# Kernel tuning notes

Measured on AMD Instinct MI355X. Metric: run time of the kernel, lower is better.

Reference implementation:

```python
import jax, jax.numpy as jnp
import numpy as np

THRESH = 0.05
MAX_PER_IMAGE = 50
NMS_THRESH = 0.3
BBOX_STD = jnp.array([0.1, 0.1, 0.2, 0.2], dtype=jnp.float32)  # TRAIN.BBOX_NORMALIZE_STDS


def _decode_boxes(rois, deltas, im_info):
    """bbox_transform_inv + clip_boxes + rescale. rois [N,5], deltas [N,4C], im_info [3]=(h,w,scale).
    Returns [N,C,4] boxes in original-image coordinates."""
    boxes = rois[:, 1:5]
    w = boxes[:, 2] - boxes[:, 0] + 1.0
    h = boxes[:, 3] - boxes[:, 1] + 1.0
    cx = boxes[:, 0] + 0.5 * w
    cy = boxes[:, 1] + 0.5 * h
    d = deltas.reshape(deltas.shape[0], -1, 4) * BBOX_STD  # [N,C,4] (unnormalize deltas)
    dx, dy, dw, dh = d[..., 0], d[..., 1], d[..., 2], d[..., 3]
    pcx = dx * w[:, None] + cx[:, None]
    pcy = dy * h[:, None] + cy[:, None]
    pw = jnp.exp(dw) * w[:, None]
    ph = jnp.exp(dh) * h[:, None]
    x1 = jnp.clip(pcx - 0.5 * pw, 0.0, im_info[1] - 1.0)
    y1 = jnp.clip(pcy - 0.5 * ph, 0.0, im_info[0] - 1.0)
    x2 = jnp.clip(pcx + 0.5 * pw, 0.0, im_info[1] - 1.0)
    y2 = jnp.clip(pcy + 0.5 * ph, 0.0, im_info[0] - 1.0)
    return jnp.stack([x1, y1, x2, y2], axis=-1) / im_info[2]


def _nms(boxes, scores, valid):
    """Greedy NMS, fixed shapes. boxes [N,4], scores [N], valid bool [N].
    Returns (boxes_sorted [N,4], kept_scores [N] with -inf for dropped)."""
    n = boxes.shape[0]
    masked = jnp.where(valid, scores, -jnp.inf)
    order = jnp.argsort(-masked)
    b = boxes[order]
    s = masked[order]
    v = valid[order]
    x1, y1, x2, y2 = b[:, 0], b[:, 1], b[:, 2], b[:, 3]
    area = (x2 - x1 + 1.0) * (y2 - y1 + 1.0)
    ix1 = jnp.maximum(x1[:, None], x1[None, :])
    iy1 = jnp.maximum(y1[:, None], y1[None, :])
    ix2 = jnp.minimum(x2[:, None], x2[None, :])
    iy2 = jnp.minimum(y2[:, None], y2[None, :])
    iw = jnp.clip(ix2 - ix1 + 1.0, 0.0)
    ih = jnp.clip(iy2 - iy1 + 1.0, 0.0)
    inter = iw * ih
    iou = inter / (area[:, None] + area[None, :] - inter)  # [N,N]

    def step(keep, i):
        suppressed = jnp.any(keep & (iou[:, i] > NMS_THRESH))
        k = v[i] & jnp.logical_not(suppressed)
        return keep.at[i].set(k), k

    keep, _ = jax.lax.scan(step, jnp.zeros((n,), dtype=bool), jnp.arange(n))
    return b, jnp.where(keep, s, -jnp.inf)


def _per_image(rois, cls_prob, bbox_pred, im_info):
    """select_boxes for one image: decode, threshold, per-class NMS, global top max_per_image.
    Returns per-class best box [C-1,4] and best score [C-1] within the capped detection set."""
    boxes = _decode_boxes(rois, bbox_pred, im_info)  # [N,C,4]
    n, c = cls_prob.shape
    fg = c - 1

    def per_class(cb, cs):
        return _nms(cb, cs, cs > THRESH)

    fb, fs = jax.vmap(per_class, in_axes=(1, 1))(boxes[:, 1:, :], cls_prob[:, 1:])  # [C-1,N,4],[C-1,N]
    flat_s = fs.reshape(-1)
    flat_b = fb.reshape(-1, 4)
    topk_s, idx = jax.lax.top_k(flat_s, MAX_PER_IMAGE)  # global cap at max_per_image
    topk_b = flat_b[idx]
    topk_cls = idx // n  # fg class id of each kept detection
    # per-class best among kept detections (used by select_box)
    onehot = topk_cls[:, None] == jnp.arange(fg)[None, :]  # [max,fg]
    per_cls = jnp.where(onehot, topk_s[:, None], -jnp.inf)  # [max,fg]
    best_s = per_cls.max(axis=0)  # [fg]
    best_b = topk_b[per_cls.argmax(axis=0)]  # [fg,4]
    return best_b, best_s


def _select_boxes(rois, cls_prob, bbox_pred, im_infos):
    return jax.lax.map(lambda t: _per_image(*t), (rois, cls_prob, bbox_pred, im_infos))


def _forward(rois_A, cls_prob_A, bbox_pred_A, im_info_A, rois_B, cls_prob_B, bbox_pred_B, im_info_B):
    bA_b, bA_s = _select_boxes(rois_A, cls_prob_A, bbox_pred_A, im_info_A)  # [B,fg,4],[B,fg]
    bB_b, bB_s = _select_boxes(rois_B, cls_prob_B, bbox_pred_B, im_info_B)
    joint = bA_s * bB_s  # class must score well in BOTH images
    cls = jnp.argmax(joint, axis=1)  # [B]
    bidx = jnp.arange(joint.shape[0])
    box_A = jax.lax.stop_gradient(bA_b[bidx, cls])
    box_B = jax.lax.stop_gradient(bB_b[bidx, cls])
    return box_A, box_B


def setup_inputs() -> dict:
    key = jax.random.key(0)
    ks = jax.random.split(key, 6)
    B, N, C = 8, 2000, 21
    H, W = 600.0, 800.0

    def make_rois(k):
        k1, k2 = jax.random.split(k)
        xy = jax.random.uniform(k1, (B, N, 2)) * jnp.array([W - 1.0, H - 1.0])
        wh = jax.random.uniform(k2, (B, N, 2), minval=8.0, maxval=300.0)
        x2y2 = jnp.minimum(xy + wh, jnp.array([W - 1.0, H - 1.0]))
        bidx = jnp.zeros((B, N, 1))
        return jnp.concatenate([bidx, xy, x2y2], axis=-1).astype(jnp.float32)

    rois_A = make_rois(ks[0])
    rois_B = make_rois(ks[1])
    cls_prob_A = jax.nn.softmax(2.0 * jax.random.normal(ks[2], (B, N, C)), axis=-1).astype(jnp.float32)
    cls_prob_B = jax.nn.softmax(2.0 * jax.random.normal(ks[3], (B, N, C)), axis=-1).astype(jnp.float32)
    bbox_pred_A = (0.2 * jax.random.normal(ks[4], (B, N, 4 * C))).astype(jnp.float32)
    bbox_pred_B = (0.2 * jax.random.normal(ks[5], (B, N, 4 * C))).astype(jnp.float32)
    im_info = jnp.tile(jnp.array([[H, W, 1.0]], dtype=jnp.float32), (B, 1))
    return dict(rois_A=rois_A, cls_prob_A=cls_prob_A, bbox_pred_A=bbox_pred_A, im_info_A=im_info,
                rois_B=rois_B, cls_prob_B=cls_prob_B, bbox_pred_B=bbox_pred_B, im_info_B=im_info)


def reference(rois_A, cls_prob_A, bbox_pred_A, im_info_A, rois_B, cls_prob_B, bbox_pred_B, im_info_B):
    return _forward(rois_A, cls_prob_A, bbox_pred_A, im_info_A,
                    rois_B, cls_prob_B, bbox_pred_B, im_info_B)
```

## Files before the change

### kernel.cpp

```cpp
#include <hip/hip_runtime.h>
#include <stdint.h>
#include <math.h>

#define BNTH 256
#define CAP 1024
#define MAXK 50
#define THRESH_F 0.05f
#define NMS_T 0.3f
#define SEGW_MAX 48

__device__ __forceinline__ void decode_box(
    const float* __restrict__ rois, const float* __restrict__ pred,
    float H, float W, float scale,
    int b, int n, int c, int N, int C, float out[4])
{
    const float* r = rois + ((size_t)b * N + n) * 5;
    float bx1 = r[1], by1 = r[2], bx2 = r[3], by2 = r[4];
    float w  = bx2 - bx1 + 1.0f;
    float h  = by2 - by1 + 1.0f;
    float cx = bx1 + 0.5f * w;
    float cy = by1 + 0.5f * h;
    const float* d = pred + ((size_t)b * N + n) * 4 * C + 4 * c;
    float dx = d[0] * 0.1f, dy = d[1] * 0.1f;
    float dw = d[2] * 0.2f, dh = d[3] * 0.2f;
    float pcx = dx * w + cx;
    float pcy = dy * h + cy;
    float pw  = expf(dw) * w;
    float ph  = expf(dh) * h;
    float X1 = fminf(fmaxf(pcx - 0.5f * pw, 0.0f), W - 1.0f);
    float Y1 = fminf(fmaxf(pcy - 0.5f * ph, 0.0f), H - 1.0f);
    float X2 = fminf(fmaxf(pcx + 0.5f * pw, 0.0f), W - 1.0f);
    float Y2 = fminf(fmaxf(pcy + 0.5f * ph, 0.0f), H - 1.0f);
    out[0] = X1 / scale;
    out[1] = Y1 / scale;
    out[2] = X2 / scale;
    out[3] = Y2 / scale;
}

template<int SN>
__device__ __forceinline__ void bitonic_desc(double* kd, int lane)
{
    constexpr int NS = SN / 64;
    #pragma unroll
    for (int k = 2; k <= SN; k <<= 1) {
        #pragma unroll
        for (int j = k >> 1; j >= 1; j >>= 1) {
            if (j >= 64) {
                const int js = j >> 6;
                #pragma unroll
                for (int s = 0; s < NS; ++s) {
                    if ((s & js) == 0) {
                        const int sp = s | js;
                        const bool d = (((s << 6) & k) == 0);
                        const double a = kd[s], bb = kd[sp];
                        kd[s]  = d ? fmax(a, bb) : fmin(a, bb);
                        kd[sp] = d ? fmin(a, bb) : fmax(a, bb);
                    }
                }
            } else {
                #pragma unroll
                for (int s = 0; s < NS; ++s) {
                    const double o = __shfl_xor(kd[s], j);
                    const bool lower = (lane & j) == 0;
                    const bool d = ((((s << 6) | lane) & k) == 0);
                    const bool takeMax = (d == lower);
                    const double mx = fmax(kd[s], o);
                    const double mn = fmin(kd[s], o);
                    kd[s] = takeMax ? mx : mn;
                }
            }
        }
    }
}

__global__ __launch_bounds__(BNTH, 1) void nms_kernel(
    const float* __restrict__ rois_A, const float* __restrict__ cls_A,
    const float* __restrict__ pred_A, const float* __restrict__ info_A,
    const float* __restrict__ rois_B, const float* __restrict__ cls_B,
    const float* __restrict__ pred_B, const float* __restrict__ info_B,
    int Bimg, int N, int C,
    float* __restrict__ kept_scores, int* __restrict__ kcounts,
    float* __restrict__ cls_box, int* __restrict__ sync_counter)
{
    const int FG = C - 1;
    const int bx = blockIdx.x;
    const int st  = bx / (Bimg * FG);
    const int rem = bx % (Bimg * FG);
    const int b = rem / FG;
    const int j = rem % FG;
    const int c = j + 1;
    const int tid = threadIdx.x;
    const int w = tid >> 6;
    const int lane = tid & 63;
    const int SEGW = (N + 63) >> 6;

    if (bx == 0 && tid == 0) *sync_counter = 0;

    const float* rois = st ? rois_B : rois_A;
    const float* cls  = st ? cls_B  : cls_A;
    const float* pred = st ? pred_B : pred_A;
    const float* info = st ? info_B : info_A;

    __shared__ uint64_t segKeys[SEGW_MAX][64];
    __shared__ int segCnt[SEGW_MAX];
    __shared__ int offL[SEGW_MAX + 1];
    __shared__ uint64_t keysL[CAP];
    __shared__ float4 boxL[CAP];
    __shared__ float  sarL[CAP];
    __shared__ float4 keptL[MAXK];

    const int ROUNDS = (SEGW + 3) >> 2;
    for (int r = 0; r < ROUNDS; ++r) {
        const int seg = w + 4 * r;
        if (seg < SEGW) {
            const int n = seg * 64 + lane;
            float sc = 0.0f;
            if (n < N) sc = cls[((size_t)b * N + n) * C + c];
            const bool val = sc > THRESH_F;
            const uint64_t bal = __ballot(val);
            if (val) {
                const int slot = __popcll(bal & ((1ull << lane) - 1ull));
                segKeys[seg][slot] =
                    ((uint64_t)__float_as_uint(sc) << 32) |
                    (uint32_t)(~(uint32_t)n);
            }
            if (lane == 0) segCnt[seg] = __popcll(bal);
        }
    }
    __syncthreads();

    if (tid < 64) {
        int v = (lane < SEGW) ? segCnt[lane] : 0;
        #pragma unroll
        for (int d = 1; d < 64; d <<= 1) {
            const int o = __shfl_up(v, d);
            if (lane >= d) v += o;
        }
        if (lane < SEGW) offL[lane + 1] = v;
        if (lane == 0) offL[0] = 0;
    }
    __syncthreads();
    const int Mfull = offL[SEGW];
    const int M = Mfull < CAP ? Mfull : CAP;

    for (int i = tid; i < CAP; i += BNTH) {
        uint64_t k = 0ull;
        if (i < M) {
            int lo = 0, hi = SEGW;
            while (hi - lo > 1) {
                const int mid = (lo + hi) >> 1;
                if (offL[mid] <= i) lo = mid; else hi = mid;
            }
            k = segKeys[lo][i - offL[lo]];
        }
        keysL[i] = k;
    }
    __syncthreads();

    if (tid < 64) {
        if (M > 1) {
            if (M <= 512) {
                double kd[8];
                #pragma unroll
                for (int s = 0; s < 8; ++s)
                    kd[s] = __longlong_as_double((long long)keysL[s * 64 + lane]);
                bitonic_desc<512>(kd, lane);
                #pragma unroll
                for (int s = 0; s < 8; ++s)
                    keysL[s * 64 + lane] = (uint64_t)__double_as_longlong(kd[s]);
            } else {
                double kd[16];
                #pragma unroll
                for (int s = 0; s < 16; ++s)
                    kd[s] = __longlong_as_double((long long)keysL[s * 64 + lane]);
                bitonic_desc<1024>(kd, lane);
                #pragma unroll
                for (int s = 0; s < 16; ++s)
                    keysL[s * 64 + lane] = (uint64_t)__double_as_longlong(kd[s]);
            }
        }
    }
    __syncthreads();

    const float H = info[b * 3 + 0];
    const float W = info[b * 3 + 1];
    const float scale = info[b * 3 + 2];
    for (int i = tid; i < M; i += BNTH) {
        const uint64_t u = keysL[i];
        const int n = (int)(~(uint32_t)u);
        float o[4];
        decode_box(rois, pred, H, W, scale, b, n, c, N, C, o);
        boxL[i] = make_float4(o[0], o[1], o[2], o[3]);
        sarL[i] = (o[2] - o[0] + 1.0f) * (o[3] - o[1] + 1.0f);
    }
    __syncthreads();

    if (tid < 64) {
        float* ksc = kept_scores + (size_t)bx * MAXK;
        int kcount = 0;
        float4 cls_best = make_float4(0.f, 0.f, 0.f, 0.f);

        for (int s = 0; s * 64 < M && kcount < MAXK; ++s) {
            const int ii = s * 64 + lane;
            const bool valid = (ii < M);
            float cx1 = 0.f, cy1 = 0.f, cx2 = 0.f, cy2 = 0.f, car = 1.0f, csc = 0.f;
            if (valid) {
                const float4 cb4 = boxL[ii];
                cx1 = cb4.x; cy1 = cb4.y; cx2 = cb4.z; cy2 = cb4.w;
                car = sarL[ii];
                csc = __uint_as_float((uint32_t)(keysL[ii] >> 32));
            }
            bool sup = !valid;
            for (int q = 0; q < kcount; ++q) {
                const float4 kb = keptL[q];
                const float kar = (kb.z - kb.x + 1.0f) * (kb.w - kb.y + 1.0f);
                const float ix1 = fmaxf(kb.x, cx1), iy1 = fmaxf(kb.y, cy1);
                const float ix2 = fminf(kb.z, cx2), iy2 = fminf(kb.w, cy2);
                const float iw = fmaxf(ix2 - ix1 + 1.0f, 0.0f);
                const float ih = fmaxf(iy2 - iy1 + 1.0f, 0.0f);
                const float inter = iw * ih;
                sup = sup || (inter / (kar + car - inter) > NMS_T);
            }
            uint64_t alive = ~__ballot(sup);
            while (alive != 0ull && kcount < MAXK) {
                const int l = __builtin_ctzll(alive);
                const float kx1 = __shfl(cx1, l), ky1 = __shfl(cy1, l);
                const float kx2 = __shfl(cx2, l), ky2 = __shfl(cy2, l);
                const float kar = (kx2 - kx1 + 1.0f) * (ky2 - ky1 + 1.0f);
                if (lane == l) {
                    keptL[kcount] = make_float4(cx1, cy1, cx2, cy2);
                    ksc[kcount] = csc;
                }
                if (kcount == 0) cls_best = make_float4(kx1, ky1, kx2, ky2);
                const float ix1 = fmaxf(kx1, cx1), iy1 = fmaxf(ky1, cy1);
                const float ix2 = fminf(kx2, cx2), iy2 = fminf(ky2, cy2);
                const float iw = fmaxf(ix2 - ix1 + 1.0f, 0.0f);
                const float ih = fmaxf(iy2 - iy1 + 1.0f, 0.0f);
                const float inter = iw * ih;
                const bool s2 = (inter / (kar + car - inter) > NMS_T);
                alive &= ~__ballot(s2);
                alive &= ~(1ull << l);
                kcount++;
            }
        }

        if (lane == 0) {
            kcounts[bx] = kcount;
            float* cbp = cls_box + (size_t)bx * 4;
            cbp[0] = cls_best.x; cbp[1] = cls_best.y;
            cbp[2] = cls_best.z; cbp[3] = cls_best.w;
        }
    }
}

__global__ __launch_bounds__(64) void select_combine(
    const float* __restrict__ kept_scores, const int* __restrict__ kcounts,
    const float* __restrict__ cls_box,
    const float* __restrict__ rois_A, const float* __restrict__ pred_A,
    const float* __restrict__ info_A,
    const float* __restrict__ rois_B, const float* __restrict__ pred_B,
    const float* __restrict__ info_B,
    int Bimg, int N, int C,
    float* best_s, float* best_b, int* sync_counter, float* __restrict__ out)
{
    const int FG = C - 1;
    const int bx = blockIdx.x;
    const int st = bx / Bimg;
    const int b  = bx % Bimg;
    const int tid = threadIdx.x;

    __shared__ float sk[20][MAXK];
    __shared__ int   skc[20];
    __shared__ float stopv[20];
    __shared__ int   cnt20[20];
    __shared__ int   inflag[20];
    __shared__ float gbox[4];
    __shared__ int   amlast;

    const size_t base = (size_t)bx * FG;
    for (int i = tid; i < FG * MAXK; i += 64)
        sk[i / MAXK][i % MAXK] = kept_scores[base * MAXK + i];
    if (tid < FG) {
        skc[tid] = kcounts[base + tid];
        cnt20[tid] = 0;
    }
    __syncthreads();
    if (tid < FG)
        stopv[tid] = (skc[tid] > 0) ? sk[tid][0] : -INFINITY;
    __syncthreads();

    for (int p = tid; p < FG * FG; p += 64) {
        const int cc = p / FG;
        const int c2 = p % FG;
        const float sc = stopv[cc];
        const int k2 = skc[c2];
        int cnt = 0;
        if (skc[cc] > 0) {
            #pragma unroll 5
            for (int k = 0; k < k2; ++k) {
                const float v = sk[c2][k];
                cnt += ((v > sc) || (v == sc && c2 < cc)) ? 1 : 0;
            }
        }
        if (cnt) atomicAdd(&cnt20[cc], cnt);
    }
    __syncthreads();
    if (tid < FG)
        inflag[tid] = (skc[tid] > 0 && cnt20[tid] < MAXK) ? 1 : 0;
    __syncthreads();

    if (tid == 0) {
        int g = -1;
        float bs = -INFINITY;
        for (int c2 = 0; c2 < FG; ++c2)
            if (skc[c2] > 0 && stopv[c2] > bs) { bs = stopv[c2]; g = c2; }
        if (g >= 0) {
            const float* cbp = cls_box + (base + g) * 4;
            gbox[0] = cbp[0]; gbox[1] = cbp[1]; gbox[2] = cbp[2]; gbox[3] = cbp[3];
        } else {
            const float* rois = st ? rois_B : rois_A;
            const float* pred = st ? pred_B : pred_A;
            const float* info = st ? info_B : info_A;
            decode_box(rois, pred, info[b * 3], info[b * 3 + 1], info[b * 3 + 2],
                       b, 0, 1, N, C, gbox);
        }
    }
    __syncthreads();

    if (tid < FG) {
        const int in = inflag[tid];
        best_s[base + tid] = in ? stopv[tid] : -INFINITY;
        float* ob = best_b + (base + tid) * 4;
        if (in) {
            const float* cbp = cls_box + (base + tid) * 4;
            ob[0] = cbp[0]; ob[1] = cbp[1]; ob[2] = cbp[2]; ob[3] = cbp[3];
        } else {
            ob[0] = gbox[0]; ob[1] = gbox[1]; ob[2] = gbox[2]; ob[3] = gbox[3];
        }
    }

    __threadfence();
    if (tid == 0) amlast = (atomicAdd(sync_counter, 1) == 2 * Bimg - 1);
    __syncthreads();
    if (amlast) {
        __threadfence();
        if (tid < Bimg) {
            const int i = tid;
            const float* sA = best_s + (size_t)i * FG;
            const float* sB = best_s + (size_t)(Bimg + i) * FG;
            float bj = 0.0f;
            int cls = 0;
            for (int cc = 0; cc < FG; ++cc) {
                const float v = sA[cc] * sB[cc];
                if (cc == 0 || v > bj) { bj = v; cls = cc; }
            }
            const float* bA = best_b + ((size_t)i * FG + cls) * 4;
            const float* bB = best_b + ((size_t)(Bimg + i) * FG + cls) * 4;
            for (int k = 0; k < 4; ++k) {
                out[i * 4 + k]            = bA[k];
                out[Bimg * 4 + i * 4 + k] = bB[k];
            }
        }
    }
}

extern "C" void kernel_launch(void* const* d_in, const int* in_sizes, int n_in,
                              void* d_out, int out_size, void* d_ws, size_t ws_size,
                              hipStream_t stream) {
    const float* rois_A = (const float*)d_in[0];
    const float* cls_A  = (const float*)d_in[1];
    const float* pred_A = (const float*)d_in[2];
    const float* info_A = (const float*)d_in[3];
    const float* rois_B = (const float*)d_in[4];
    const float* cls_B  = (const float*)d_in[5];
    const float* pred_B = (const float*)d_in[6];
    const float* info_B = (const float*)d_in[7];
    float* out = (float*)d_out;

    const int Bimg = in_sizes[3] / 3;
    const int N    = in_sizes[0] / (Bimg * 5);
    const int C    = in_sizes[1] / (Bimg * N);
    const int FG   = C - 1;
    const int NSB  = 2 * Bimg * FG;

    char* ws = (char*)d_ws;
    int* sync_counter = (int*)ws;
    size_t off = 256;
    float* kept_scores = (float*)(ws + off);
    off += (size_t)NSB * MAXK * sizeof(float);
    int* kcounts = (int*)(ws + off);
    off += (size_t)NSB * sizeof(int);
    float* cls_box = (float*)(ws + off);
    off += (size_t)NSB * 4 * sizeof(float);
    float* best_s = (float*)(ws + off);
    off += (size_t)NSB * sizeof(float);
    float* best_b = (float*)(ws + off);

    nms_kernel<<<NSB, BNTH, 0, stream>>>(
        rois_A, cls_A, pred_A, info_A,
        rois_B, cls_B, pred_B, info_B,
        Bimg, N, C, kept_scores, kcounts, cls_box, sync_counter);

    select_combine<<<2 * Bimg, 64, 0, stream>>>(
        kept_scores, kcounts, cls_box,
        rois_A, pred_A, info_A, rois_B, pred_B, info_B,
        Bimg, N, C, best_s, best_b, sync_counter, out);
}
```

Baseline: 60.48 us.

## Fuse select-combine into NMS kernel, replace bitonic with rank sort, bitmask NMS

Removes the second kernel launch by having the last block, chosen with a monotonic ticket counter, run the cross-class selection and final combine from shared memory. The single-wavefront bitonic sort is replaced by an all-thread rank (counting) sort. Greedy NMS within each 64-candidate chunk now precomputes a 64-bit suppression mask per lane and resolves keeps with readlane. Score loads are hoisted into registers before the ballot compaction. The ticket-modulo scheme avoids a reset but assumes the workspace counter starts at a multiple of the grid size, and the O(M^2) rank sort can be costly when many candidates pass the threshold.

```diff
diff --git a/kernel.cpp b/kernel.cpp
--- a/kernel.cpp
+++ b/kernel.cpp
@@ -7,7 +7,10 @@
 #define MAXK 50
 #define THRESH_F 0.05f
 #define NMS_T 0.3f
-#define SEGW_MAX 48
+#define SEGW_MAX 32
+#define RMAX 8
+#define FG_MAX 24
+#define NIMG_MAX 32
 
 __device__ __forceinline__ void decode_box(
     const float* __restrict__ rois, const float* __restrict__ pred,
@@ -37,42 +40,6 @@
     out[3] = Y2 / scale;
 }
 
-template<int SN>
-__device__ __forceinline__ void bitonic_desc(double* kd, int lane)
-{
-    constexpr int NS = SN / 64;
-    #pragma unroll
-    for (int k = 2; k <= SN; k <<= 1) {
-        #pragma unroll
-        for (int j = k >> 1; j >= 1; j >>= 1) {
-            if (j >= 64) {
-                const int js = j >> 6;
-                #pragma unroll
-                for (int s = 0; s < NS; ++s) {
-                    if ((s & js) == 0) {
-                        const int sp = s | js;
-                        const bool d = (((s << 6) & k) == 0);
-                        const double a = kd[s], bb = kd[sp];
-                        kd[s]  = d ? fmax(a, bb) : fmin(a, bb);
-                        kd[sp] = d ? fmin(a, bb) : fmax(a, bb);
-                    }
-                }
-            } else {
-                #pragma unroll
-                for (int s = 0; s < NS; ++s) {
-                    const double o = __shfl_xor(kd[s], j);
-                    const bool lower = (lane & j) == 0;
-                    const bool d = ((((s << 6) | lane) & k) == 0);
-                    const bool takeMax = (d == lower);
-                    const double mx = fmax(kd[s], o);
-                    const double mn = fmin(kd[s], o);
-                    kd[s] = takeMax ? mx : mn;
-                }
-            }
-        }
-    }
-}
-
 __global__ __launch_bounds__(BNTH, 1) void nms_kernel(
     const float* __restrict__ rois_A, const float* __restrict__ cls_A,
     const float* __restrict__ pred_A, const float* __restrict__ info_A,
@@ -80,7 +47,8 @@
     const float* __restrict__ pred_B, const float* __restrict__ info_B,
     int Bimg, int N, int C,
     float* __restrict__ kept_scores, int* __restrict__ kcounts,
-    float* __restrict__ cls_box, int* __restrict__ sync_counter)
+    float* __restrict__ cls_box,
+    unsigned long long* __restrict__ ticket, float* __restrict__ out)
 {
     const int FG = C - 1;
     const int bx = blockIdx.x;
@@ -94,8 +62,6 @@
     const int lane = tid & 63;
     const int SEGW = (N + 63) >> 6;
 
-    if (bx == 0 && tid == 0) *sync_counter = 0;
-
     const float* rois = st ? rois_B : rois_A;
     const float* cls  = st ? cls_B  : cls_A;
     const float* pred = st ? pred_B : pred_A;
@@ -108,20 +74,36 @@
     __shared__ float4 boxL[CAP];
     __shared__ float  sarL[CAP];
     __shared__ float4 keptL[MAXK];
-
-    const int ROUNDS = (SEGW + 3) >> 2;
-    for (int r = 0; r < ROUNDS; ++r) {
+    __shared__ float  keptSc[MAXK];
+    __shared__ int amlastL;
+    __shared__ float swSc[4][FG_MAX];
+    __shared__ int   swKc[4][FG_MAX];
+    __shared__ int   swCnt[4][FG_MAX];
+    __shared__ float bestSL[NIMG_MAX][FG_MAX];
+    __shared__ float4 bestBL[NIMG_MAX][FG_MAX];
+
+    uint64_t* sortedK = &segKeys[0][0];
+
+    float scv[RMAX];
+    #pragma unroll
+    for (int r = 0; r < RMAX; ++r) {
+        const int seg = w + 4 * r;
+        const int n = seg * 64 + lane;
+        scv[r] = 0.0f;
+        if (seg < SEGW && n < N)
+            scv[r] = cls[((size_t)b * N + n) * C + c];
+    }
+    #pragma unroll
+    for (int r = 0; r < RMAX; ++r) {
         const int seg = w + 4 * r;
         if (seg < SEGW) {
             const int n = seg * 64 + lane;
-            float sc = 0.0f;
-            if (n < N) sc = cls[((size_t)b * N + n) * C + c];
-            const bool val = sc > THRESH_F;
+            const bool val = scv[r] > THRESH_F;
             const uint64_t bal = __ballot(val);
             if (val) {
                 const int slot = __popcll(bal & ((1ull << lane) - 1ull));
                 segKeys[seg][slot] =
-                    ((uint64_t)__float_as_uint(sc) << 32) |
+                    ((uint64_t)__float_as_uint(scv[r]) << 32) |
                     (uint32_t)(~(uint32_t)n);
             }
             if (lane == 0) segCnt[seg] = __popcll(bal);
@@ -157,28 +139,33 @@
     }
     __syncthreads();
 
-    if (tid < 64) {
-        if (M > 1) {
-            if (M <= 512) {
-                double kd[8];
-                #pragma unroll
-                for (int s = 0; s < 8; ++s)
-                    kd[s] = __longlong_as_double((long long)keysL[s * 64 + lane]);
-                bitonic_desc<512>(kd, lane);
-                #pragma unroll
-                for (int s = 0; s < 8; ++s)
-                    keysL[s * 64 + lane] = (uint64_t)__double_as_longlong(kd[s]);
-            } else {
-                double kd[16];
-                #pragma unroll
-                for (int s = 0; s < 16; ++s)
-                    kd[s] = __longlong_as_double((long long)keysL[s * 64 + lane]);
-                bitonic_desc<1024>(kd, lane);
-                #pragma unroll
-                for (int s = 0; s < 16; ++s)
-                    keysL[s * 64 + lane] = (uint64_t)__double_as_longlong(kd[s]);
-            }
-        }
+    {
+        const double d0 = __longlong_as_double((long long)keysL[tid]);
+        const double d1 = __longlong_as_double((long long)keysL[tid + 256]);
+        const double d2 = __longlong_as_double((long long)keysL[tid + 512]);
+        const double d3 = __longlong_as_double((long long)keysL[tid + 768]);
+        int r0 = 0, r1 = 0, r2 = 0, r3 = 0;
+        if (M <= 512) {
+            #pragma unroll 4
+            for (int jj = 0; jj < M; ++jj) {
+                const double dj = __longlong_as_double((long long)keysL[jj]);
+                r0 += (dj > d0) ? 1 : 0;
+                r1 += (dj > d1) ? 1 : 0;
+            }
+        } else {
+            #pragma unroll 4
+            for (int jj = 0; jj < M; ++jj) {
+                const double dj = __longlong_as_double((long long)keysL[jj]);
+                r0 += (dj > d0) ? 1 : 0;
+                r1 += (dj > d1) ? 1 : 0;
+                r2 += (dj > d2) ? 1 : 0;
+                r3 += (dj > d3) ? 1 : 0;
+            }
+        }
+        if (tid < M)       sortedK[r0] = (uint64_t)__double_as_longlong(d0);
+        if (tid + 256 < M) sortedK[r1] = (uint64_t)__double_as_longlong(d1);
+        if (tid + 512 < M) sortedK[r2] = (uint64_t)__double_as_longlong(d2);
+        if (tid + 768 < M) sortedK[r3] = (uint64_t)__double_as_longlong(d3);
     }
     __syncthreads();
 
@@ -186,7 +173,7 @@
     const float W = info[b * 3 + 1];
     const float scale = info[b * 3 + 2];
     for (int i = tid; i < M; i += BNTH) {
-        const uint64_t u = keysL[i];
+        const uint64_t u = sortedK[i];
         const int n = (int)(~(uint32_t)u);
         float o[4];
         decode_box(rois, pred, H, W, scale, b, n, c, N, C, o);
@@ -196,21 +183,20 @@
     __syncthreads();
 
     if (tid < 64) {
-        float* ksc = kept_scores + (size_t)bx * MAXK;
         int kcount = 0;
-        float4 cls_best = make_float4(0.f, 0.f, 0.f, 0.f);
-
         for (int s = 0; s * 64 < M && kcount < MAXK; ++s) {
             const int ii = s * 64 + lane;
             const bool valid = (ii < M);
-            float cx1 = 0.f, cy1 = 0.f, cx2 = 0.f, cy2 = 0.f, car = 1.0f, csc = 0.f;
+            float cx1 = 0.f, cy1 = 0.f, cx2 = 0.f, cy2 = 0.f;
+            float car = 1.0f, csc = 0.f;
             if (valid) {
                 const float4 cb4 = boxL[ii];
                 cx1 = cb4.x; cy1 = cb4.y; cx2 = cb4.z; cy2 = cb4.w;
                 car = sarL[ii];
-                csc = __uint_as_float((uint32_t)(keysL[ii] >> 32));
+                csc = __uint_as_float((uint32_t)(sortedK[ii] >> 32));
             }
             bool sup = !valid;
+            #pragma unroll 4
             for (int q = 0; q < kcount; ++q) {
                 const float4 kb = keptL[q];
                 const float kar = (kb.z - kb.x + 1.0f) * (kb.w - kb.y + 1.0f);
@@ -221,146 +207,135 @@
                 const float inter = iw * ih;
                 sup = sup || (inter / (kar + car - inter) > NMS_T);
             }
-            uint64_t alive = ~__ballot(sup);
-            while (alive != 0ull && kcount < MAXK) {
-                const int l = __builtin_ctzll(alive);
-                const float kx1 = __shfl(cx1, l), ky1 = __shfl(cy1, l);
-                const float kx2 = __shfl(cx2, l), ky2 = __shfl(cy2, l);
-                const float kar = (kx2 - kx1 + 1.0f) * (ky2 - ky1 + 1.0f);
-                if (lane == l) {
-                    keptL[kcount] = make_float4(cx1, cy1, cx2, cy2);
-                    ksc[kcount] = csc;
-                }
-                if (kcount == 0) cls_best = make_float4(kx1, ky1, kx2, ky2);
-                const float ix1 = fmaxf(kx1, cx1), iy1 = fmaxf(ky1, cy1);
-                const float ix2 = fminf(kx2, cx2), iy2 = fminf(ky2, cy2);
+            uint64_t smask = 0ull;
+            #pragma unroll 16
+            for (int jj = 0; jj < 64; ++jj) {
+                const float4 bj = boxL[s * 64 + jj];
+                const float jar = sarL[s * 64 + jj];
+                const float ix1 = fmaxf(cx1, bj.x), iy1 = fmaxf(cy1, bj.y);
+                const float ix2 = fminf(cx2, bj.z), iy2 = fminf(cy2, bj.w);
                 const float iw = fmaxf(ix2 - ix1 + 1.0f, 0.0f);
                 const float ih = fmaxf(iy2 - iy1 + 1.0f, 0.0f);
                 const float inter = iw * ih;
-                const bool s2 = (inter / (kar + car - inter) > NMS_T);
-                alive &= ~__ballot(s2);
+                const float iou = inter / (car + jar - inter);
+                smask |= (iou > NMS_T) ? (1ull << jj) : 0ull;
+            }
+            const uint32_t mlo = (uint32_t)smask;
+            const uint32_t mhi = (uint32_t)(smask >> 32);
+
+            uint64_t alive = __ballot(valid && !sup);
+            while (alive != 0ull && kcount < MAXK) {
+                int l = __builtin_ctzll(alive);
+                l = __builtin_amdgcn_readfirstlane(l);
+                const uint32_t klo = (uint32_t)__builtin_amdgcn_readlane((int)mlo, l);
+                const uint32_t khi = (uint32_t)__builtin_amdgcn_readlane((int)mhi, l);
+                const uint64_t ml = ((uint64_t)khi << 32) | klo;
+                if (lane == l) {
+                    keptL[kcount] = make_float4(cx1, cy1, cx2, cy2);
+                    keptSc[kcount] = csc;
+                }
+                alive &= ~ml;
                 alive &= ~(1ull << l);
                 kcount++;
             }
         }
-
+        if (lane < kcount) kept_scores[(size_t)bx * MAXK + lane] = keptSc[lane];
         if (lane == 0) {
             kcounts[bx] = kcount;
-            float* cbp = cls_box + (size_t)bx * 4;
-            cbp[0] = cls_best.x; cbp[1] = cls_best.y;
-            cbp[2] = cls_best.z; cbp[3] = cls_best.w;
-        }
-    }
-}
-
-__global__ __launch_bounds__(64) void select_combine(
-    const float* __restrict__ kept_scores, const int* __restrict__ kcounts,
-    const float* __restrict__ cls_box,
-    const float* __restrict__ rois_A, const float* __restrict__ pred_A,
-    const float* __restrict__ info_A,
-    const float* __restrict__ rois_B, const float* __restrict__ pred_B,
-    const float* __restrict__ info_B,
-    int Bimg, int N, int C,
-    float* best_s, float* best_b, int* sync_counter, float* __restrict__ out)
-{
-    const int FG = C - 1;
-    const int bx = blockIdx.x;
-    const int st = bx / Bimg;
-    const int b  = bx % Bimg;
-    const int tid = threadIdx.x;
-
-    __shared__ float sk[20][MAXK];
-    __shared__ int   skc[20];
-    __shared__ float stopv[20];
-    __shared__ int   cnt20[20];
-    __shared__ int   inflag[20];
-    __shared__ float gbox[4];
-    __shared__ int   amlast;
-
-    const size_t base = (size_t)bx * FG;
-    for (int i = tid; i < FG * MAXK; i += 64)
-        sk[i / MAXK][i % MAXK] = kept_scores[base * MAXK + i];
-    if (tid < FG) {
-        skc[tid] = kcounts[base + tid];
-        cnt20[tid] = 0;
-    }
-    __syncthreads();
-    if (tid < FG)
-        stopv[tid] = (skc[tid] > 0) ? sk[tid][0] : -INFINITY;
-    __syncthreads();
-
-    for (int p = tid; p < FG * FG; p += 64) {
-        const int cc = p / FG;
-        const int c2 = p % FG;
-        const float sc = stopv[cc];
-        const int k2 = skc[c2];
-        int cnt = 0;
-        if (skc[cc] > 0) {
-            #pragma unroll 5
-            for (int k = 0; k < k2; ++k) {
-                const float v = sk[c2][k];
-                cnt += ((v > sc) || (v == sc && c2 < cc)) ? 1 : 0;
-            }
-        }
-        if (cnt) atomicAdd(&cnt20[cc], cnt);
-    }
-    __syncthreads();
-    if (tid < FG)
-        inflag[tid] = (skc[tid] > 0 && cnt20[tid] < MAXK) ? 1 : 0;
-    __syncthreads();
-
+            float4 cb = (kcount > 0) ? keptL[0] : make_float4(0.f, 0.f, 0.f, 0.f);
+            *(float4*)(cls_box + (size_t)bx * 4) = cb;
+        }
+    }
+    __syncthreads();
+
+    __threadfence();
     if (tid == 0) {
-        int g = -1;
-        float bs = -INFINITY;
-        for (int c2 = 0; c2 < FG; ++c2)
-            if (skc[c2] > 0 && stopv[c2] > bs) { bs = stopv[c2]; g = c2; }
-        if (g >= 0) {
-            const float* cbp = cls_box + (base + g) * 4;
-            gbox[0] = cbp[0]; gbox[1] = cbp[1]; gbox[2] = cbp[2]; gbox[3] = cbp[3];
+        const unsigned long long t = atomicAdd(ticket, 1ull);
+        amlastL = ((t % (unsigned long long)gridDim.x) ==
+                   (unsigned long long)(gridDim.x - 1)) ? 1 : 0;
+    }
+    __syncthreads();
+    if (!amlastL) return;
+    __threadfence();
+
+    const int nimg = 2 * Bimg;
+    for (int img = w; img < nimg; img += 4) {
+        int kc_l = 0; float sv_l = -INFINITY;
+        if (lane < FG) {
+            kc_l = kcounts[img * FG + lane];
+            if (kc_l > 0) sv_l = kept_scores[((size_t)img * FG + lane) * MAXK];
+            swKc[w][lane] = kc_l;
+            swSc[w][lane] = sv_l;
+            swCnt[w][lane] = 0;
+        }
+        for (int p = lane; p < FG * FG; p += 64) {
+            const int cc = p / FG, c2 = p % FG;
+            const float sc = swSc[w][cc];
+            const int k2 = swKc[w][c2];
+            int cnt = 0;
+            if (swKc[w][cc] > 0) {
+                const float* kp = kept_scores + ((size_t)img * FG + c2) * MAXK;
+                for (int k = 0; k < k2; ++k) {
+                    const float v = kp[k];
+                    const bool greater = (v > sc) || (v == sc && c2 < cc);
+                    if (!greater) break;
+                    cnt++;
+                }
+            }
+            if (cnt) atomicAdd(&swCnt[w][cc], cnt);
+        }
+        uint32_t mu = 0u;
+        if (lane < FG && kc_l > 0) {
+            const uint32_t bb = __float_as_uint(sv_l);
+            mu = (bb & 0x80000000u) ? ~bb : (bb | 0x80000000u);
+        }
+        uint64_t gkey = (mu == 0u) ? 0ull
+                        : (((uint64_t)mu << 8) | (uint64_t)(255 - lane));
+        #pragma unroll
+        for (int m = 1; m < 64; m <<= 1) {
+            const uint64_t o = __shfl_xor(gkey, m);
+            if (o > gkey) gkey = o;
+        }
+        float4 gbox;
+        if ((gkey >> 8) != 0ull) {
+            const int g = 255 - (int)(gkey & 0xFFull);
+            gbox = *(const float4*)(cls_box + ((size_t)img * FG + g) * 4);
         } else {
-            const float* rois = st ? rois_B : rois_A;
-            const float* pred = st ? pred_B : pred_A;
-            const float* info = st ? info_B : info_A;
-            decode_box(rois, pred, info[b * 3], info[b * 3 + 1], info[b * 3 + 2],
-                       b, 0, 1, N, C, gbox);
-        }
-    }
-    __syncthreads();
-
-    if (tid < FG) {
-        const int in = inflag[tid];
-        best_s[base + tid] = in ? stopv[tid] : -INFINITY;
-        float* ob = best_b + (base + tid) * 4;
-        if (in) {
-            const float* cbp = cls_box + (base + tid) * 4;
-            ob[0] = cbp[0]; ob[1] = cbp[1]; ob[2] = cbp[2]; ob[3] = cbp[3];
-        } else {
-            ob[0] = gbox[0]; ob[1] = gbox[1]; ob[2] = gbox[2]; ob[3] = gbox[3];
-        }
-    }
-
-    __threadfence();
-    if (tid == 0) amlast = (atomicAdd(sync_counter, 1) == 2 * Bimg - 1);
-    __syncthreads();
-    if (amlast) {
-        __threadfence();
-        if (tid < Bimg) {
-            const int i = tid;
-            const float* sA = best_s + (size_t)i * FG;
-            const float* sB = best_s + (size_t)(Bimg + i) * FG;
-            float bj = 0.0f;
-            int cls = 0;
-            for (int cc = 0; cc < FG; ++cc) {
-                const float v = sA[cc] * sB[cc];
-                if (cc == 0 || v > bj) { bj = v; cls = cc; }
-            }
-            const float* bA = best_b + ((size_t)i * FG + cls) * 4;
-            const float* bB = best_b + ((size_t)(Bimg + i) * FG + cls) * 4;
-            for (int k = 0; k < 4; ++k) {
-                out[i * 4 + k]            = bA[k];
-                out[Bimg * 4 + i * 4 + k] = bB[k];
-            }
-        }
+            const int st2 = img >= Bimg;
+            const int b2  = img - st2 * Bimg;
+            const float* rois2 = st2 ? rois_B : rois_A;
+            const float* pred2 = st2 ? pred_B : pred_A;
+            const float* info2 = st2 ? info_B : info_A;
+            float o[4];
+            decode_box(rois2, pred2, info2[b2 * 3], info2[b2 * 3 + 1],
+                       info2[b2 * 3 + 2], b2, 0, 1, N, C, o);
+            gbox = make_float4(o[0], o[1], o[2], o[3]);
+        }
+        if (lane < FG) {
+            const int total = swCnt[w][lane];
+            const bool in = (kc_l > 0 && total < MAXK);
+            bestSL[img][lane] = in ? sv_l : -INFINITY;
+            bestBL[img][lane] = in
+                ? *(const float4*)(cls_box + ((size_t)img * FG + lane) * 4)
+                : gbox;
+        }
+    }
+    __syncthreads();
+
+    if (tid < Bimg) {
+        const int i = tid;
+        float bj = 0.0f;
+        int cls_ = 0;
+        for (int cc = 0; cc < FG; ++cc) {
+            const float v = bestSL[i][cc] * bestSL[Bimg + i][cc];
+            if (cc == 0 || v > bj) { bj = v; cls_ = cc; }
+        }
+        const float4 bA = bestBL[i][cls_];
+        const float4 bB = bestBL[Bimg + i][cls_];
+        out[i * 4 + 0] = bA.x; out[i * 4 + 1] = bA.y;
+        out[i * 4 + 2] = bA.z; out[i * 4 + 3] = bA.w;
+        out[Bimg * 4 + i * 4 + 0] = bB.x; out[Bimg * 4 + i * 4 + 1] = bB.y;
+        out[Bimg * 4 + i * 4 + 2] = bB.z; out[Bimg * 4 + i * 4 + 3] = bB.w;
     }
 }
 
@@ -384,25 +359,16 @@
     const int NSB  = 2 * Bimg * FG;
 
     char* ws = (char*)d_ws;
-    int* sync_counter = (int*)ws;
+    unsigned long long* ticket = (unsigned long long*)ws;
     size_t off = 256;
     float* kept_scores = (float*)(ws + off);
     off += (size_t)NSB * MAXK * sizeof(float);
     int* kcounts = (int*)(ws + off);
     off += (size_t)NSB * sizeof(int);
     float* cls_box = (float*)(ws + off);
-    off += (size_t)NSB * 4 * sizeof(float);
-    float* best_s = (float*)(ws + off);
-    off += (size_t)NSB * sizeof(float);
-    float* best_b = (float*)(ws + off);
 
     nms_kernel<<<NSB, BNTH, 0, stream>>>(
         rois_A, cls_A, pred_A, info_A,
         rois_B, cls_B, pred_B, info_B,
-        Bimg, N, C, kept_scores, kcounts, cls_box, sync_counter);
-
-    select_combine<<<2 * Bimg, 64, 0, stream>>>(
-        kept_scores, kcounts, cls_box,
-        rois_A, pred_A, info_A, rois_B, pred_B, info_B,
-        Bimg, N, C, best_s, best_b, sync_counter, out);
+        Bimg, N, C, kept_scores, kcounts, cls_box, ticket, out);
 }
```

New measurement: 89.84 us. 1.49x slower.
